# Performance work log

Measured on AMD Instinct MI355X. Metric: run time of the kernel, lower is better.

The kernel has to match this reference:

```python
import jax, jax.numpy as jnp
import numpy as np

N_NODES = 50000
N_EDGES = 800000
D = 512
N_LAYERS = 3
LN_EPS = 1e-5


def _layer_norm(h, gamma, beta):
    mu = jnp.mean(h, axis=-1, keepdims=True)
    var = jnp.mean(jnp.square(h - mu), axis=-1, keepdims=True)
    return (h - mu) * jax.lax.rsqrt(var + LN_EPS) * gamma + beta


def setup_inputs() -> dict:
    key = jax.random.key(0)
    ks = jax.random.split(key, 5)
    x = jax.random.normal(ks[0], (N_NODES, D), dtype=jnp.float32)
    edge_index = jax.random.randint(ks[1], (2, N_EDGES), 0, N_NODES, dtype=jnp.int64)
    edge_weight = jax.random.uniform(ks[2], (N_EDGES,), dtype=jnp.float32)
    # GCNConv lin weights (xavier-ish scale), zero biases; LayerNorm affine params
    Ws = jax.random.normal(ks[3], (N_LAYERS, D, D), dtype=jnp.float32) * (1.0 / np.sqrt(D))
    bs = jnp.zeros((N_LAYERS, D), dtype=jnp.float32)
    gammas = jnp.ones((N_LAYERS, D), dtype=jnp.float32)
    betas = jnp.zeros((N_LAYERS, D), dtype=jnp.float32)
    return {"x": x, "edge_index": edge_index, "edge_weight": edge_weight,
            "Ws": Ws, "bs": bs, "gammas": gammas, "betas": betas}


def reference(x, edge_index, edge_weight, Ws, bs, gammas, betas):
    n = x.shape[0]
    row, col = edge_index[0], edge_index[1]  # source -> target (PyG convention)
    # add self loops with weight 1 (GCNConv add_self_loops=True)
    sl = jnp.arange(n, dtype=edge_index.dtype)
    row2 = jnp.concatenate([row, sl])
    col2 = jnp.concatenate([col, sl])
    ew = jnp.concatenate([edge_weight, jnp.ones((n,), dtype=edge_weight.dtype)])
    # symmetric normalization: D^{-1/2} A D^{-1/2}
    deg = jax.ops.segment_sum(ew, col2, num_segments=n)
    dinv = jnp.where(deg > 0, 1.0 / jnp.sqrt(jnp.where(deg > 0, deg, 1.0)), 0.0)
    norm = dinv[row2] * ew * dinv[col2]  # [E+N]

    for i in range(N_LAYERS):
        identity = x
        h = x @ Ws[i].T                       # [N, D] linear transform
        msg = norm[:, None] * h[row2]         # gather + scale per edge
        agg = jax.ops.segment_sum(msg, col2, num_segments=n) + bs[i]
        h = _layer_norm(agg, gammas[i], betas[i])
        if i < N_LAYERS - 1:
            h = jax.nn.relu(h)                # dropout=0 -> identity
        x = h + identity                      # residual (dims equal -> Identity proj)
    return x
```

## Files before the change

### kernel.cpp

```cpp
#include <hip/hip_runtime.h>
#include <hip/hip_bf16.h>
#include <stdint.h>

#define D 512
#define LN_EPS 1e-5f

typedef __attribute__((ext_vector_type(8))) short bf16x8;
typedef __attribute__((ext_vector_type(4))) float f32x4;

__device__ __forceinline__ unsigned short f32_to_bf16_bits(float x) {
    unsigned int u = __float_as_uint(x);
    u += 0x7fffu + ((u >> 16) & 1u);
    return (unsigned short)(u >> 16);
}
__device__ __forceinline__ float bf16lo(unsigned int u) { return __uint_as_float(u << 16); }
__device__ __forceinline__ float bf16hi(unsigned int u) { return __uint_as_float(u & 0xffff0000u); }

typedef const __attribute__((address_space(1))) unsigned int GU;
typedef __attribute__((address_space(3))) unsigned int LU;
__device__ __forceinline__ void gload_lds16(const void* g, void* l) {
    __builtin_amdgcn_global_load_lds((GU*)g, (LU*)l, 16, 0, 0);
}

__global__ void k_init(float* deg, int* cnt, int n) {
    int i = blockIdx.x * blockDim.x + threadIdx.x;
    if (i < n) { deg[i] = 1.0f; cnt[i] = 1; }
}

__global__ void k_deg_cnt(const int* __restrict__ col, const float* __restrict__ ew,
                          float* deg, int* cnt, int E) {
    int e = blockIdx.x * blockDim.x + threadIdx.x;
    if (e < E) {
        int c = col[e];
        atomicAdd(&deg[c], ew[e]);
        atomicAdd(&cnt[c], 1);
    }
}

__global__ __launch_bounds__(1024) void k_scan(const int* __restrict__ cnt,
                                               float* __restrict__ deg,
                                               int* __restrict__ rptr,
                                               int* __restrict__ cur, int n) {
    for (int i = threadIdx.x; i < n; i += 1024) deg[i] = rsqrtf(deg[i]);

    const int tid = threadIdx.x, lane = tid & 63, wv = tid >> 6;
    const int chunk = (n + 15) >> 4;
    const int wbeg = wv * chunk;
    const int wend = min(wbeg + chunk, n);

    int tot = 0;
    for (int i = wbeg + lane; i < wend; i += 64) tot += cnt[i];
#pragma unroll
    for (int off = 32; off > 0; off >>= 1) tot += __shfl_xor(tot, off);
    __shared__ int woff[17];
    if (lane == 0) woff[wv] = tot;
    __syncthreads();
    if (tid == 0) {
        int r = 0;
        for (int w = 0; w < 16; ++w) { int t = woff[w]; woff[w] = r; r += t; }
        woff[16] = r;
    }
    __syncthreads();

    int run = woff[wv];
    for (int base = wbeg; base < wend; base += 64) {
        int i = base + lane;
        int v = (i < wend) ? cnt[i] : 0;
        int inc = v;
#pragma unroll
        for (int off = 1; off < 64; off <<= 1) {
            int u = __shfl_up(inc, off);
            if (lane >= off) inc += u;
        }
        if (i < wend) {
            int excl = run + inc - v;
            rptr[i] = excl;
            cur[i] = excl;
        }
        run += __shfl(inc, 63);
    }
    if (tid == 0) rptr[n] = woff[16];
}

__global__ void k_fill(const int* __restrict__ row, const int* __restrict__ col,
                       const float* __restrict__ ew, const float* __restrict__ dinv,
                       int* cur, uint2* __restrict__ srcval, int N, int E) {
    int i = blockIdx.x * blockDim.x + threadIdx.x;
    if (i < N) {
        int slot = atomicAdd(&cur[i], 1);
        float d = dinv[i];
        uint2 sv; sv.x = (unsigned)i; sv.y = __float_as_uint(d * d);
        srcval[slot] = sv;
    } else if (i < N + E) {
        int e = i - N;
        int r = row[e], c = col[e];
        int slot = atomicAdd(&cur[c], 1);
        uint2 sv; sv.x = (unsigned)r;
        sv.y = __float_as_uint(dinv[r] * ew[e] * dinv[c]);
        srcval[slot] = sv;
    }
}

__global__ void k_cast4(const float4* __restrict__ in, ushort4* __restrict__ out,
                        long n4, long nin4) {
    long i = (long)blockIdx.x * blockDim.x + threadIdx.x;
    if (i >= n4) return;
    float4 v;
    if (i < nin4) v = in[i];
    else { v.x = 0.f; v.y = 0.f; v.z = 0.f; v.w = 0.f; }
    ushort4 o;
    o.x = f32_to_bf16_bits(v.x);
    o.y = f32_to_bf16_bits(v.y);
    o.z = f32_to_bf16_bits(v.z);
    o.w = f32_to_bf16_bits(v.w);
    out[i] = o;
}

__global__ __launch_bounds__(256) void k_gemm(
    const short* __restrict__ A,
    const short* __restrict__ W,
    short* __restrict__ H,
    int Mpad) {
    __shared__ short As[128 * 32];
    __shared__ short Bs[128 * 32];
    const int tid = threadIdx.x;
    const int wave = tid >> 6, lane = tid & 63;
    const int wm = (wave >> 1) * 64, wn = (wave & 1) * 64;
    const int tm = blockIdx.x * 128, tn = blockIdx.y * 128;
    f32x4 acc[4][4] = {};
    const int fr = lane & 15, fc = lane >> 4;

    const int r0 = tid >> 2, cb0 = (tid & 3) * 8;
    const short* Ab = A + (size_t)(tm + r0) * 512 + cb0;
    const short* Wb = W + (size_t)(tn + r0) * 512 + cb0;

    for (int k0 = 0; k0 < 512; k0 += 32) {
        gload_lds16(Ab + k0,                    &As[tid * 8]);
        gload_lds16(Ab + (size_t)64 * 512 + k0, &As[(tid + 256) * 8]);
        gload_lds16(Wb + k0,                    &Bs[tid * 8]);
        gload_lds16(Wb + (size_t)64 * 512 + k0, &Bs[(tid + 256) * 8]);
        __syncthreads();
        bf16x8 af[4], bfr[4];
#pragma unroll
        for (int m = 0; m < 4; ++m)
            af[m] = *(const bf16x8*)&As[(wm + m * 16 + fr) * 32 + fc * 8];
#pragma unroll
        for (int n = 0; n < 4; ++n)
            bfr[n] = *(const bf16x8*)&Bs[(wn + n * 16 + fr) * 32 + fc * 8];
#pragma unroll
        for (int m = 0; m < 4; ++m) {
#pragma unroll
            for (int n = 0; n < 4; ++n)
                acc[m][n] = __builtin_amdgcn_mfma_f32_16x16x32_bf16(af[m], bfr[n], acc[m][n], 0, 0, 0);
        }
        __syncthreads();
    }
    const int cbase = tn + wn + (lane & 15);
    const int rbase = tm + wm + fc * 4;
#pragma unroll
    for (int m = 0; m < 4; ++m) {
#pragma unroll
        for (int n = 0; n < 4; ++n) {
#pragma unroll
            for (int j = 0; j < 4; ++j) {
                int r = rbase + m * 16 + j;
                int c = cbase + n * 16;
                H[(size_t)r * 512 + c] = (short)f32_to_bf16_bits(acc[m][n][j]);
            }
        }
    }
}

__global__ __launch_bounds__(256) void k_agg_ln(
    const uint4* __restrict__ H4,
    const int* __restrict__ rptr,
    const uint2* __restrict__ srcval,
    const float4* __restrict__ bias,
    const float4* __restrict__ gamma,
    const float4* __restrict__ beta,
    uint4* __restrict__ xb,
    float4* __restrict__ out_f32,
    int N, int last) {
    const int wv = threadIdx.x >> 6, lane = threadIdx.x & 63;
    const int t = blockIdx.x * 4 + wv;
    if (t >= N) return;
    const int beg = rptr[t], end = rptr[t + 1];

    float a[8], b[8];
#pragma unroll
    for (int i = 0; i < 8; ++i) { a[i] = 0.f; b[i] = 0.f; }

    for (int base = beg; base < end; base += 64) {
        int m = end - base;
        if (m > 64) m = 64;
        int idx = base + lane;
        if (idx > end - 1) idx = end - 1;
        uint2 svl = srcval[idx];
        int e = 0;
        for (; e + 2 <= m; e += 2) {
            unsigned s0 = __shfl(svl.x, e);
            unsigned s1 = __shfl(svl.x, e + 1);
            float w0 = __uint_as_float(__shfl(svl.y, e));
            float w1 = __uint_as_float(__shfl(svl.y, e + 1));
            uint4 u0 = H4[(size_t)s0 * 64 + lane];
            uint4 u1 = H4[(size_t)s1 * 64 + lane];
            a[0] = fmaf(w0, bf16lo(u0.x), a[0]);
            a[1] = fmaf(w0, bf16hi(u0.x), a[1]);
            a[2] = fmaf(w0, bf16lo(u0.y), a[2]);
            a[3] = fmaf(w0, bf16hi(u0.y), a[3]);
            a[4] = fmaf(w0, bf16lo(u0.z), a[4]);
            a[5] = fmaf(w0, bf16hi(u0.z), a[5]);
            a[6] = fmaf(w0, bf16lo(u0.w), a[6]);
            a[7] = fmaf(w0, bf16hi(u0.w), a[7]);
            b[0] = fmaf(w1, bf16lo(u1.x), b[0]);
            b[1] = fmaf(w1, bf16hi(u1.x), b[1]);
            b[2] = fmaf(w1, bf16lo(u1.y), b[2]);
            b[3] = fmaf(w1, bf16hi(u1.y), b[3]);
            b[4] = fmaf(w1, bf16lo(u1.z), b[4]);
            b[5] = fmaf(w1, bf16hi(u1.z), b[5]);
            b[6] = fmaf(w1, bf16lo(u1.w), b[6]);
            b[7] = fmaf(w1, bf16hi(u1.w), b[7]);
        }
        if (e < m) {
            unsigned s0 = __shfl(svl.x, e);
            float w0 = __uint_as_float(__shfl(svl.y, e));
            uint4 u0 = H4[(size_t)s0 * 64 + lane];
            a[0] = fmaf(w0, bf16lo(u0.x), a[0]);
            a[1] = fmaf(w0, bf16hi(u0.x), a[1]);
            a[2] = fmaf(w0, bf16lo(u0.y), a[2]);
            a[3] = fmaf(w0, bf16hi(u0.y), a[3]);
            a[4] = fmaf(w0, bf16lo(u0.z), a[4]);
            a[5] = fmaf(w0, bf16hi(u0.z), a[5]);
            a[6] = fmaf(w0, bf16lo(u0.w), a[6]);
            a[7] = fmaf(w0, bf16hi(u0.w), a[7]);
        }
    }
#pragma unroll
    for (int i = 0; i < 8; ++i) a[i] += b[i];

    float4 bv0 = bias[lane * 2], bv1 = bias[lane * 2 + 1];
    a[0] += bv0.x; a[1] += bv0.y; a[2] += bv0.z; a[3] += bv0.w;
    a[4] += bv1.x; a[5] += bv1.y; a[6] += bv1.z; a[7] += bv1.w;

    float s1 = 0.f, s2 = 0.f;
#pragma unroll
    for (int i = 0; i < 8; ++i) { s1 += a[i]; s2 += a[i] * a[i]; }
#pragma unroll
    for (int off = 32; off > 0; off >>= 1) {
        s1 += __shfl_xor(s1, off);
        s2 += __shfl_xor(s2, off);
    }
    const float mean = s1 * (1.0f / 512.0f);
    const float var = s2 * (1.0f / 512.0f) - mean * mean;
    const float rstd = rsqrtf(var + LN_EPS);

    float4 gv0 = gamma[lane * 2], gv1 = gamma[lane * 2 + 1];
    float4 bt0 = beta[lane * 2], bt1 = beta[lane * 2 + 1];
    float o[8];
    o[0] = (a[0] - mean) * rstd * gv0.x + bt0.x;
    o[1] = (a[1] - mean) * rstd * gv0.y + bt0.y;
    o[2] = (a[2] - mean) * rstd * gv0.z + bt0.z;
    o[3] = (a[3] - mean) * rstd * gv0.w + bt0.w;
    o[4] = (a[4] - mean) * rstd * gv1.x + bt1.x;
    o[5] = (a[5] - mean) * rstd * gv1.y + bt1.y;
    o[6] = (a[6] - mean) * rstd * gv1.z + bt1.z;
    o[7] = (a[7] - mean) * rstd * gv1.w + bt1.w;
    if (!last) {
#pragma unroll
        for (int i = 0; i < 8; ++i) o[i] = fmaxf(o[i], 0.f);
    }
    uint4 idu = xb[(size_t)t * 64 + lane];
    o[0] += bf16lo(idu.x); o[1] += bf16hi(idu.x);
    o[2] += bf16lo(idu.y); o[3] += bf16hi(idu.y);
    o[4] += bf16lo(idu.z); o[5] += bf16hi(idu.z);
    o[6] += bf16lo(idu.w); o[7] += bf16hi(idu.w);

    if (last) {
        float4 f0, f1;
        f0.x = o[0]; f0.y = o[1]; f0.z = o[2]; f0.w = o[3];
        f1.x = o[4]; f1.y = o[5]; f1.z = o[6]; f1.w = o[7];
        out_f32[(size_t)t * 128 + lane * 2] = f0;
        out_f32[(size_t)t * 128 + lane * 2 + 1] = f1;
    } else {
        uint4 pk;
        pk.x = ((unsigned)f32_to_bf16_bits(o[1]) << 16) | f32_to_bf16_bits(o[0]);
        pk.y = ((unsigned)f32_to_bf16_bits(o[3]) << 16) | f32_to_bf16_bits(o[2]);
        pk.z = ((unsigned)f32_to_bf16_bits(o[5]) << 16) | f32_to_bf16_bits(o[4]);
        pk.w = ((unsigned)f32_to_bf16_bits(o[7]) << 16) | f32_to_bf16_bits(o[6]);
        xb[(size_t)t * 64 + lane] = pk;
    }
}

extern "C" void kernel_launch(void* const* d_in, const int* in_sizes, int n_in,
                              void* d_out, int out_size, void* d_ws, size_t ws_size,
                              hipStream_t stream) {
    const float* x0     = (const float*)d_in[0];
    const int*   ei     = (const int*)d_in[1];
    const float* ew     = (const float*)d_in[2];
    const float* Ws     = (const float*)d_in[3];
    const float* bs     = (const float*)d_in[4];
    const float* gammas = (const float*)d_in[5];
    const float* betas  = (const float*)d_in[6];

    const int N = in_sizes[0] / D;
    const int E = in_sizes[1] / 2;
    const int L = in_sizes[3] / (D * D);
    const int Mpad = (N + 127) & ~127;

    char* p = (char*)d_ws;
    auto carve = [&](size_t bytes) {
        char* q = p;
        p += (bytes + 255) & ~(size_t)255;
        return (void*)q;
    };
    short* xb     = (short*)carve((size_t)Mpad * D * 2);
    short* hb     = (short*)carve((size_t)Mpad * D * 2);
    short* wb     = (short*)carve((size_t)L * D * D * 2);
    float* dinv   = (float*)carve((size_t)N * 4);
    int*   cnt    = (int*)carve((size_t)N * 4);
    int*   rptr   = (int*)carve((size_t)(N + 1) * 4);
    int*   cur    = (int*)carve((size_t)N * 4);
    uint2* srcval = (uint2*)carve((size_t)(E + N) * 8);
    (void)ws_size; (void)n_in; (void)out_size;

    const int* rowI = ei;
    const int* colI = ei + E;

    const int nbN = (N + 255) / 256;
    const int nbE = (E + 255) / 256;
    const int nbF = (N + E + 255) / 256;

    k_init<<<nbN, 256, 0, stream>>>(dinv, cnt, N);
    k_deg_cnt<<<nbE, 256, 0, stream>>>(colI, ew, dinv, cnt, E);
    k_scan<<<1, 1024, 0, stream>>>(cnt, dinv, rptr, cur, N);
    k_fill<<<nbF, 256, 0, stream>>>(rowI, colI, ew, dinv, cur, srcval, N, E);

    {
        long n4 = (long)L * D * D / 4;
        k_cast4<<<(int)((n4 + 255) / 256), 256, 0, stream>>>(
            (const float4*)Ws, (ushort4*)wb, n4, n4);
    }
    {
        long n4 = (long)Mpad * D / 4, nin4 = (long)N * D / 4;
        k_cast4<<<(int)((n4 + 255) / 256), 256, 0, stream>>>(
            (const float4*)x0, (ushort4*)xb, n4, nin4);
    }

    for (int l = 0; l < L; ++l) {
        dim3 g(Mpad / 128, D / 128);
        k_gemm<<<g, 256, 0, stream>>>(xb, wb + (size_t)l * D * D, hb, Mpad);
        int last = (l == L - 1);
        k_agg_ln<<<(N + 3) / 4, 256, 0, stream>>>(
            (const uint4*)hb, rptr, srcval,
            (const float4*)(bs + (size_t)l * D),
            (const float4*)(gammas + (size_t)l * D),
            (const float4*)(betas + (size_t)l * D),
            (uint4*)xb, (float4*)d_out, N, last);
    }
}
```

Measured before the change: 734.0 us.

## Fuse prep kernels, widen GEMM tile to 128x256, use nontemporal output stores

Merges the init, weight cast and input cast kernels into a single prep launch to cut launch overhead. Widens the GEMM block to 512 threads covering a 128x256 output tile, so each A tile is reused across more columns. Switches the aggregation/LayerNorm output stores to nontemporal stores so streamed outputs do not pollute the cache. The larger GEMM tile halves the number of blocks in that dimension and raises LDS use per block, which may reduce occupancy.

```diff
diff --git a/kernel.cpp b/kernel.cpp
--- a/kernel.cpp
+++ b/kernel.cpp
@@ -7,6 +7,7 @@
 
 typedef __attribute__((ext_vector_type(8))) short bf16x8;
 typedef __attribute__((ext_vector_type(4))) float f32x4;
+typedef __attribute__((ext_vector_type(4))) unsigned int u32x4;
 
 __device__ __forceinline__ unsigned short f32_to_bf16_bits(float x) {
     unsigned int u = __float_as_uint(x);
@@ -22,9 +23,34 @@
     __builtin_amdgcn_global_load_lds((GU*)g, (LU*)l, 16, 0, 0);
 }
 
-__global__ void k_init(float* deg, int* cnt, int n) {
-    int i = blockIdx.x * blockDim.x + threadIdx.x;
-    if (i < n) { deg[i] = 1.0f; cnt[i] = 1; }
+__global__ void k_prep(const float4* __restrict__ x0, ushort4* __restrict__ xb4,
+                       const float4* __restrict__ Ws4, ushort4* __restrict__ wb4,
+                       float* __restrict__ deg, int* __restrict__ cnt,
+                       long nx4, long nxin4, long nw4, int N) {
+    long id = (long)blockIdx.x * blockDim.x + threadIdx.x;
+    if (id < nx4) {
+        float4 v;
+        if (id < nxin4) v = x0[id];
+        else { v.x = 0.f; v.y = 0.f; v.z = 0.f; v.w = 0.f; }
+        ushort4 o;
+        o.x = f32_to_bf16_bits(v.x);
+        o.y = f32_to_bf16_bits(v.y);
+        o.z = f32_to_bf16_bits(v.z);
+        o.w = f32_to_bf16_bits(v.w);
+        xb4[id] = o;
+    } else if (id < nx4 + nw4) {
+        long i = id - nx4;
+        float4 v = Ws4[i];
+        ushort4 o;
+        o.x = f32_to_bf16_bits(v.x);
+        o.y = f32_to_bf16_bits(v.y);
+        o.z = f32_to_bf16_bits(v.z);
+        o.w = f32_to_bf16_bits(v.w);
+        wb4[i] = o;
+    } else {
+        long i = id - nx4 - nw4;
+        if (i < N) { deg[i] = 1.0f; cnt[i] = 1; }
+    }
 }
 
 __global__ void k_deg_cnt(const int* __restrict__ col, const float* __restrict__ ew,
@@ -101,32 +127,17 @@
     }
 }
 
-__global__ void k_cast4(const float4* __restrict__ in, ushort4* __restrict__ out,
-                        long n4, long nin4) {
-    long i = (long)blockIdx.x * blockDim.x + threadIdx.x;
-    if (i >= n4) return;
-    float4 v;
-    if (i < nin4) v = in[i];
-    else { v.x = 0.f; v.y = 0.f; v.z = 0.f; v.w = 0.f; }
-    ushort4 o;
-    o.x = f32_to_bf16_bits(v.x);
-    o.y = f32_to_bf16_bits(v.y);
-    o.z = f32_to_bf16_bits(v.z);
-    o.w = f32_to_bf16_bits(v.w);
-    out[i] = o;
-}
-
-__global__ __launch_bounds__(256) void k_gemm(
+__global__ __launch_bounds__(512) void k_gemm(
     const short* __restrict__ A,
     const short* __restrict__ W,
     short* __restrict__ H,
     int Mpad) {
     __shared__ short As[128 * 32];
-    __shared__ short Bs[128 * 32];
+    __shared__ short Bs[256 * 32];
     const int tid = threadIdx.x;
     const int wave = tid >> 6, lane = tid & 63;
-    const int wm = (wave >> 1) * 64, wn = (wave & 1) * 64;
-    const int tm = blockIdx.x * 128, tn = blockIdx.y * 128;
+    const int wm = (wave >> 2) * 64, wn = (wave & 3) * 64;
+    const int tm = blockIdx.x * 128, tn = blockIdx.y * 256;
     f32x4 acc[4][4] = {};
     const int fr = lane & 15, fc = lane >> 4;
 
@@ -135,10 +146,9 @@
     const short* Wb = W + (size_t)(tn + r0) * 512 + cb0;
 
     for (int k0 = 0; k0 < 512; k0 += 32) {
-        gload_lds16(Ab + k0,                    &As[tid * 8]);
-        gload_lds16(Ab + (size_t)64 * 512 + k0, &As[(tid + 256) * 8]);
-        gload_lds16(Wb + k0,                    &Bs[tid * 8]);
-        gload_lds16(Wb + (size_t)64 * 512 + k0, &Bs[(tid + 256) * 8]);
+        gload_lds16(Ab + k0,                     &As[tid * 8]);
+        gload_lds16(Wb + k0,                     &Bs[tid * 8]);
+        gload_lds16(Wb + (size_t)128 * 512 + k0, &Bs[(tid + 512) * 8]);
         __syncthreads();
         bf16x8 af[4], bfr[4];
 #pragma unroll
@@ -276,18 +286,19 @@
     o[6] += bf16lo(idu.w); o[7] += bf16hi(idu.w);
 
     if (last) {
-        float4 f0, f1;
-        f0.x = o[0]; f0.y = o[1]; f0.z = o[2]; f0.w = o[3];
-        f1.x = o[4]; f1.y = o[5]; f1.z = o[6]; f1.w = o[7];
-        out_f32[(size_t)t * 128 + lane * 2] = f0;
-        out_f32[(size_t)t * 128 + lane * 2 + 1] = f1;
+        f32x4 f0, f1;
+        f0[0] = o[0]; f0[1] = o[1]; f0[2] = o[2]; f0[3] = o[3];
+        f1[0] = o[4]; f1[1] = o[5]; f1[2] = o[6]; f1[3] = o[7];
+        f32x4* dst = (f32x4*)&out_f32[(size_t)t * 128 + lane * 2];
+        __builtin_nontemporal_store(f0, dst);
+        __builtin_nontemporal_store(f1, dst + 1);
     } else {
-        uint4 pk;
-        pk.x = ((unsigned)f32_to_bf16_bits(o[1]) << 16) | f32_to_bf16_bits(o[0]);
-        pk.y = ((unsigned)f32_to_bf16_bits(o[3]) << 16) | f32_to_bf16_bits(o[2]);
-        pk.z = ((unsigned)f32_to_bf16_bits(o[5]) << 16) | f32_to_bf16_bits(o[4]);
-        pk.w = ((unsigned)f32_to_bf16_bits(o[7]) << 16) | f32_to_bf16_bits(o[6]);
-        xb[(size_t)t * 64 + lane] = pk;
+        u32x4 pk;
+        pk[0] = ((unsigned)f32_to_bf16_bits(o[1]) << 16) | f32_to_bf16_bits(o[0]);
+        pk[1] = ((unsigned)f32_to_bf16_bits(o[3]) << 16) | f32_to_bf16_bits(o[2]);
+        pk[2] = ((unsigned)f32_to_bf16_bits(o[5]) << 16) | f32_to_bf16_bits(o[4]);
+        pk[3] = ((unsigned)f32_to_bf16_bits(o[7]) << 16) | f32_to_bf16_bits(o[6]);
+        __builtin_nontemporal_store(pk, (u32x4*)&xb[(size_t)t * 64 + lane]);
     }
 }
 
@@ -326,29 +337,21 @@
     const int* rowI = ei;
     const int* colI = ei + E;
 
-    const int nbN = (N + 255) / 256;
-    const int nbE = (E + 255) / 256;
-    const int nbF = (N + E + 255) / 256;
-
-    k_init<<<nbN, 256, 0, stream>>>(dinv, cnt, N);
-    k_deg_cnt<<<nbE, 256, 0, stream>>>(colI, ew, dinv, cnt, E);
+    {
+        long nx4 = (long)Mpad * D / 4, nxin4 = (long)N * D / 4;
+        long nw4 = (long)L * D * D / 4;
+        long tot = nx4 + nw4 + N;
+        k_prep<<<(int)((tot + 255) / 256), 256, 0, stream>>>(
+            (const float4*)x0, (ushort4*)xb, (const float4*)Ws, (ushort4*)wb,
+            dinv, cnt, nx4, nxin4, nw4, N);
+    }
+    k_deg_cnt<<<(E + 255) / 256, 256, 0, stream>>>(colI, ew, dinv, cnt, E);
     k_scan<<<1, 1024, 0, stream>>>(cnt, dinv, rptr, cur, N);
-    k_fill<<<nbF, 256, 0, stream>>>(rowI, colI, ew, dinv, cur, srcval, N, E);
-
-    {
-        long n4 = (long)L * D * D / 4;
-        k_cast4<<<(int)((n4 + 255) / 256), 256, 0, stream>>>(
-            (const float4*)Ws, (ushort4*)wb, n4, n4);
-    }
-    {
-        long n4 = (long)Mpad * D / 4, nin4 = (long)N * D / 4;
-        k_cast4<<<(int)((n4 + 255) / 256), 256, 0, stream>>>(
-            (const float4*)x0, (ushort4*)xb, n4, nin4);
-    }
+    k_fill<<<(N + E + 255) / 256, 256, 0, stream>>>(rowI, colI, ew, dinv, cur, srcval, N, E);
 
     for (int l = 0; l < L; ++l) {
-        dim3 g(Mpad / 128, D / 128);
-        k_gemm<<<g, 256, 0, stream>>>(xb, wb + (size_t)l * D * D, hb, Mpad);
+        dim3 g(Mpad / 128, D / 256);
+        k_gemm<<<g, 512, 0, stream>>>(xb, wb + (size_t)l * D * D, hb, Mpad);
         int last = (l == L - 1);
         k_agg_ln<<<(N + 3) / 4, 256, 0, stream>>>(
             (const uint4*)hb, rptr, srcval,
```

Result: faster. 705.4 us (-3.9%).
